# Performance work log

Hardware: AMD Instinct MI355X
Metric: run time of the kernel (lower is better)

The kernel has to match this reference:

```python
import jax, jax.numpy as jnp
import numpy as np

N_NODES = 100000
N_EDGES = 3200000
BN_EPS = 1e-5


def setup_inputs() -> dict:
    key = jax.random.key(0)
    ks = jax.random.split(key, 16)
    return {
        "x": jax.random.normal(ks[0], (N_NODES, 2), jnp.float32),
        "eq_labels": jax.random.randint(ks[1], (N_NODES,), 0, 32, jnp.int32),
        "edge_index": jax.random.randint(ks[2], (2, N_EDGES), 0, N_NODES, jnp.int32),
        "eq_emb": jax.random.normal(ks[3], (32, 8), jnp.float32),
        "W1_0": jax.random.normal(ks[4], (10, 64), jnp.float32) * 0.3,
        "b1_0": jnp.zeros((64,), jnp.float32),
        "W2_0": jax.random.normal(ks[5], (64, 64), jnp.float32) * 0.12,
        "b2_0": jnp.zeros((64,), jnp.float32),
        "eps_0": jnp.zeros((), jnp.float32),
        "gamma_0": jnp.ones((64,), jnp.float32),
        "beta_0": jnp.zeros((64,), jnp.float32),
        "W1_s": jax.random.normal(ks[6], (2, 64, 64), jnp.float32) * 0.12,
        "b1_s": jnp.zeros((2, 64), jnp.float32),
        "W2_s": jax.random.normal(ks[7], (2, 64, 64), jnp.float32) * 0.12,
        "b2_s": jnp.zeros((2, 64), jnp.float32),
        "eps_s": jnp.zeros((2,), jnp.float32),
        "gamma_s": jnp.ones((2, 64), jnp.float32),
        "beta_s": jnp.zeros((2, 64), jnp.float32),
        "Wf": jax.random.normal(ks[8], (64, 1), jnp.float32) * 0.12,
        "bf": jnp.zeros((1,), jnp.float32),
    }


def _gin_bn_relu(h, src, dst, W1, b1, W2, b2, eps, gamma, beta):
    # GINConv: (1+eps)*x_i + sum_{j->i} x_j, then 2-layer ReLU MLP, then BN, ReLU
    agg = jax.ops.segment_sum(h[src], dst, num_segments=N_NODES)
    h = (1.0 + eps) * h + agg
    h = jax.nn.relu(h @ W1 + b1)
    h = jax.nn.relu(h @ W2 + b2)
    mu = jnp.mean(h, axis=0)
    var = jnp.var(h, axis=0)
    h = (h - mu) * jax.lax.rsqrt(var + BN_EPS) * gamma + beta
    return jax.nn.relu(h)


def reference(x, eq_labels, edge_index, eq_emb, W1_0, b1_0, W2_0, b2_0, eps_0,
              gamma_0, beta_0, W1_s, b1_s, W2_s, b2_s, eps_s, gamma_s, beta_s,
              Wf, bf):
    src, dst = edge_index[0], edge_index[1]
    h = jnp.concatenate([x, eq_emb[eq_labels]], axis=-1)  # [N, 10]
    h = _gin_bn_relu(h, src, dst, W1_0, b1_0, W2_0, b2_0, eps_0, gamma_0, beta_0)
    for i in range(2):
        h = _gin_bn_relu(h, src, dst, W1_s[i], b1_s[i], W2_s[i], b2_s[i],
                         eps_s[i], gamma_s[i], beta_s[i])
    return (h @ Wf + bf).squeeze(-1)  # [N]
```

## Files before the change

### kernel.cpp

```cpp
#include <hip/hip_runtime.h>

#define N_NODES 100000
#define N_EDGES 3200000
#define BN_EPS 1e-5f

#define BLK_NODES 128
#define NBLK 782
#define CHUNK 16384
#define NW ((N_EDGES + CHUNK - 1) / CHUNK)
#define BCAP 4480
#define CUR_PAD 16
#define NSLICE 32

typedef unsigned int uint;
typedef unsigned short ushort;
typedef _Float16 half_t;
typedef __attribute__((ext_vector_type(8))) _Float16 h8v;
typedef __attribute__((ext_vector_type(4))) float f4v;

__device__ inline float bf_lo(uint u) { return __uint_as_float(u << 16); }
__device__ inline float bf_hi(uint u) { return __uint_as_float(u & 0xffff0000u); }
__device__ inline float h_lo(uint u) {
    union { ushort s; half_t h; } r; r.s = (ushort)(u & 0xffffu); return (float)r.h;
}
__device__ inline float h_hi(uint u) {
    union { ushort s; half_t h; } r; r.s = (ushort)(u >> 16); return (float)r.h;
}
__device__ inline ushort f2bf(float a) {
    uint ua = __float_as_uint(a); ua += 0x7fffu + ((ua >> 16) & 1u);
    return (ushort)(ua >> 16);
}
__device__ inline ushort f2h(float a) {
    union { half_t h; ushort u; } r;
    r.h = (half_t)a;
    return r.u;
}
__device__ inline uint packh2(float a, float b) {
    return (uint)f2h(a) | ((uint)f2h(b) << 16);
}
__device__ inline h8v loadH(const ushort* p) {
    union { uint4 q; h8v f; } r;
    r.q = *(const uint4*)p;
    return r.f;
}
__device__ inline h8v loadHh(const half_t* p) {
    union { uint4 q; h8v f; } r;
    r.q = *(const uint4*)p;
    return r.f;
}
__device__ inline f4v mfma16(h8v a, h8v b, f4v c) {
    return __builtin_amdgcn_mfma_f32_16x16x32_f16(a, b, c, 0, 0, 0);
}

#define FETCH_COLS(rr, st, dg, mx, wv, wv2)                                   \
    {                                                                         \
        int _r = (rr);                                                        \
        st = __shfl(myStart, 2 * _r + hl, 64);                                \
        dg = __shfl(myDeg, 2 * _r + hl, 64);                                  \
        int _dA = __shfl(myDeg, 2 * _r, 64);                                  \
        int _dB = __shfl(myDeg, 2 * _r + 1, 64);                              \
        mx = max(_dA, _dB);                                                   \
        int _e1 = min(l5, dg - 1); _e1 = _e1 < 0 ? 0 : _e1;                   \
        int _e2 = min(32 + l5, dg - 1); _e2 = _e2 < 0 ? 0 : _e2;              \
        wv = col[st + _e1];                                                   \
        wv2 = col[st + _e2];                                                  \
    }

__global__ __launch_bounds__(256) void k_h0(const float* __restrict__ x,
                                            const int* __restrict__ lab,
                                            const float* __restrict__ emb,
                                            ushort* __restrict__ h0,
                                            const float* __restrict__ W1_0,
                                            const float* __restrict__ W2_0,
                                            const float* __restrict__ W1_s,
                                            const float* __restrict__ W2_s,
                                            ushort* __restrict__ W0t,
                                            ushort* __restrict__ W20t,
                                            ushort* __restrict__ Wst, int n) {
    int i = blockIdx.x * blockDim.x + threadIdx.x;
    if (i < n) {
        float v[16];
        v[0] = x[2 * i];
        v[1] = x[2 * i + 1];
        int L = lab[i];
#pragma unroll
        for (int k = 0; k < 8; k++) v[2 + k] = emb[L * 8 + k];
#pragma unroll
        for (int k = 10; k < 16; k++) v[k] = 0.f;
        uint o8[8];
#pragma unroll
        for (int k = 0; k < 8; k++) o8[k] = packh2(v[2 * k], v[2 * k + 1]);
        uint4* o = (uint4*)(h0 + (size_t)i * 16);
        o[0] = uint4{o8[0], o8[1], o8[2], o8[3]};
        o[1] = uint4{o8[4], o8[5], o8[6], o8[7]};
    }
    if (blockIdx.x == 0) {
        int t = threadIdx.x;
        for (int j = t; j < 64 * 32; j += 256) {
            int nn = j >> 5, k = j & 31;
            W0t[j] = (k < 10) ? f2h(W1_0[k * 64 + nn]) : (ushort)0;
        }
        for (int j = t; j < 4096; j += 256) {
            int nn = j >> 6, k = j & 63;
            W20t[j] = f2h(W2_0[k * 64 + nn]);
        }
        for (int l = 0; l < 2; l++) {
            const float* w1 = W1_s + l * 4096;
            const float* w2 = W2_s + l * 4096;
            for (int j = t; j < 4096; j += 256) {
                int nn = j >> 6, k = j & 63;
                Wst[l * 8192 + j] = f2h(w1[k * 64 + nn]);
                Wst[l * 8192 + 4096 + j] = f2h(w2[k * 64 + nn]);
            }
        }
    }
}

__global__ __launch_bounds__(256) void k_fill(const int* __restrict__ src,
                                              const int* __restrict__ dst,
                                              int* __restrict__ gcur,
                                              int* __restrict__ bucket) {
    __shared__ int cnt[NBLK];
    __shared__ int off[NBLK];
    int t = threadIdx.x;
    for (int b = t; b < NBLK; b += 256) cnt[b] = 0;
    __syncthreads();
    int my0 = blockIdx.x * CHUNK + t * 64;
    for (int k = 0; k < 64; k += 4) {
        int e = my0 + k;
        if (e + 3 < N_EDGES) {
            int4 d4 = *(const int4*)(dst + e);
            atomicAdd(&cnt[d4.x >> 7], 1);
            atomicAdd(&cnt[d4.y >> 7], 1);
            atomicAdd(&cnt[d4.z >> 7], 1);
            atomicAdd(&cnt[d4.w >> 7], 1);
        } else {
#pragma unroll
            for (int kk = 0; kk < 4; kk++) {
                int ee = e + kk;
                if (ee < N_EDGES) atomicAdd(&cnt[dst[ee] >> 7], 1);
            }
        }
    }
    __syncthreads();
    for (int b = t; b < NBLK; b += 256) {
        int c = cnt[b];
        off[b] = (c > 0) ? atomicAdd(&gcur[b * CUR_PAD], c) : 0;
    }
    __syncthreads();
    for (int k = 0; k < 64; k += 4) {
        int e = my0 + k;
        if (e + 3 < N_EDGES) {
            int4 d4 = *(const int4*)(dst + e);
            int4 s4 = *(const int4*)(src + e);
            int dd[4] = {d4.x, d4.y, d4.z, d4.w};
            int ss[4] = {s4.x, s4.y, s4.z, s4.w};
#pragma unroll
            for (int kk = 0; kk < 4; kk++) {
                int b = dd[kk] >> 7;
                int p = atomicAdd(&off[b], 1);
                if (p < BCAP)
                    bucket[(size_t)b * BCAP + p] = ((dd[kk] & 127) << 17) | ss[kk];
            }
        } else {
#pragma unroll
            for (int kk = 0; kk < 4; kk++) {
                int ee = e + kk;
                if (ee < N_EDGES) {
                    int d = dst[ee], s = src[ee];
                    int b = d >> 7;
                    int p = atomicAdd(&off[b], 1);
                    if (p < BCAP)
                        bucket[(size_t)b * BCAP + p] = ((d & 127) << 17) | s;
                }
            }
        }
    }
}

__global__ __launch_bounds__(256) void k_sort(const int* __restrict__ gcur,
                                              const int* __restrict__ bucket,
                                              int* __restrict__ col2,
                                              int2* __restrict__ nodeoff, int n) {
    __shared__ int cnt[BLK_NODES];
    __shared__ int scn[BLK_NODES];
    __shared__ int cur[BLK_NODES];
    int t = threadIdx.x;
    int blk = blockIdx.x;
    if (t < BLK_NODES) cnt[t] = 0;
    __syncthreads();
    int cc = min(gcur[blk * CUR_PAD], BCAP);
    const int* bb = bucket + (size_t)blk * BCAP;
    for (int i = t; i < cc; i += 256) atomicAdd(&cnt[bb[i] >> 17], 1);
    __syncthreads();
    if (t < BLK_NODES) scn[t] = cnt[t];
    __syncthreads();
#pragma unroll
    for (int off = 1; off < BLK_NODES; off <<= 1) {
        int v = (t >= off && t < BLK_NODES) ? scn[t - off] : 0;
        __syncthreads();
        if (t < BLK_NODES) scn[t] += v;
        __syncthreads();
    }
    if (t < BLK_NODES) {
        int start = scn[t] - cnt[t];
        cur[t] = start;
        int node = blk * BLK_NODES + t;
        if (node < n) nodeoff[node] = int2{blk * BCAP + start, cnt[t]};
    }
    __syncthreads();
    int* out = col2 + (size_t)blk * BCAP;
    for (int i = t; i < cc; i += 256) {
        int w = bb[i];
        int p = atomicAdd(&cur[w >> 17], 1);
        out[p] = w & 0x1FFFF;
    }
}

__global__ __launch_bounds__(256, 4) void k_layer0M(const ushort* __restrict__ h0,
                                                    const int2* __restrict__ nodeoff,
                                                    const int* __restrict__ col,
                                                    const float* __restrict__ epsp,
                                                    const ushort* __restrict__ W0t,
                                                    const float* __restrict__ b1,
                                                    const ushort* __restrict__ W20t,
                                                    const float* __restrict__ b2,
                                                    ushort* __restrict__ hraw,
                                                    float* __restrict__ part_out) {
    __shared__ half_t buf[4][16][72];
    int t = threadIdx.x, w = t >> 6, lane = t & 63;
    int base = blockIdx.x * 64 + w * 16;
    float ep = 1.f + *epsp;
    int hl = lane >> 5, l5 = lane & 31;
    int q = l5 & 3, g = l5 >> 2;
    const uint* hb = (const uint*)h0;

    int nj = base + (lane & 15);
    int2 no2 = nodeoff[nj];
    bool njv = nj < N_NODES;
    int myStart = njv ? no2.x : 0;
    int myDeg = njv ? no2.y : 0;

    int stC, dgC, mxC, wvC, wv2C;
    int stN, dgN, mxN, wvN, wv2N;
    FETCH_COLS(0, stC, dgC, mxC, wvC, wv2C);
    FETCH_COLS(1, stN, dgN, mxN, wvN, wv2N);

    for (int r = 0; r < 8; r++) {
        int stNN, dgNN, mxNN, wvNN, wv2NN;
        FETCH_COLS(min(r + 2, 7), stNN, dgNN, mxNN, wvNN, wv2NN);
        int deg = dgC, mx = mxC;
        float ac[4] = {0.f, 0.f, 0.f, 0.f};
        if (mx > 0) {
            int idx[4];
#pragma unroll
            for (int i = 0; i < 4; i++) idx[i] = __shfl(wvC, (hl << 5) + g + 8 * i, 64);
            uint2 rows[4];
#pragma unroll
            for (int i = 0; i < 4; i++)
                rows[i] = *(const uint2*)(hb + (size_t)idx[i] * 8 + q * 2);
#pragma unroll
            for (int i = 0; i < 4; i++) {
                float m = (g + 8 * i < deg) ? 1.f : 0.f;
                ac[0] = fmaf(m, h_lo(rows[i].x), ac[0]);
                ac[1] = fmaf(m, h_hi(rows[i].x), ac[1]);
                ac[2] = fmaf(m, h_lo(rows[i].y), ac[2]);
                ac[3] = fmaf(m, h_hi(rows[i].y), ac[3]);
            }
            if (mx > 32) {
                int idx2[4];
#pragma unroll
                for (int i = 0; i < 4; i++) idx2[i] = __shfl(wv2C, (hl << 5) + g + 8 * i, 64);
                uint2 rows2[4];
#pragma unroll
                for (int i = 0; i < 4; i++)
                    rows2[i] = *(const uint2*)(hb + (size_t)idx2[i] * 8 + q * 2);
#pragma unroll
                for (int i = 0; i < 4; i++) {
                    float m = (32 + g + 8 * i < deg) ? 1.f : 0.f;
                    ac[0] = fmaf(m, h_lo(rows2[i].x), ac[0]);
                    ac[1] = fmaf(m, h_hi(rows2[i].x), ac[1]);
                    ac[2] = fmaf(m, h_lo(rows2[i].y), ac[2]);
                    ac[3] = fmaf(m, h_hi(rows2[i].y), ac[3]);
                }
                for (int e = 64 + g; e < deg; e += 8) {
                    uint2 v = *(const uint2*)(hb + (size_t)col[stC + e] * 8 + q * 2);
                    ac[0] += h_lo(v.x); ac[1] += h_hi(v.x);
                    ac[2] += h_lo(v.y); ac[3] += h_hi(v.y);
                }
            }
        }
#pragma unroll
        for (int o = 4; o < 32; o <<= 1) {
#pragma unroll
            for (int k = 0; k < 4; k++) ac[k] += __shfl_xor(ac[k], o, 64);
        }
        int node = base + 2 * r + hl;
        bool valid = node < N_NODES;
        int nodeC = valid ? node : 0;
        float vm = valid ? ep : 0.f;
        uint2 sv = *(const uint2*)(hb + (size_t)nodeC * 8 + q * 2);
        ac[0] = fmaf(vm, h_lo(sv.x), ac[0]);
        ac[1] = fmaf(vm, h_hi(sv.x), ac[1]);
        ac[2] = fmaf(vm, h_lo(sv.y), ac[2]);
        ac[3] = fmaf(vm, h_hi(sv.y), ac[3]);
        if (!valid) { ac[0] = ac[1] = ac[2] = ac[3] = 0.f; }
        if (g == 0) {
            int nl = 2 * r + hl;
            *(uint2*)&buf[w][nl][q * 4] = uint2{packh2(ac[0], ac[1]), packh2(ac[2], ac[3])};
            *(uint2*)&buf[w][nl][16 + q * 4] = uint2{0u, 0u};
        }
        stC = stN; dgC = dgN; mxC = mxN; wvC = wvN; wv2C = wv2N;
        stN = stNN; dgN = dgNN; mxN = mxNN; wvN = wvNN; wv2N = wv2NN;
    }
    int mr = lane & 15, kq = lane >> 4, nc = lane & 15;
    h8v A0 = loadHh(&buf[w][mr][kq * 8]);
#pragma unroll
    for (int nt = 0; nt < 4; nt++) {
        float bb = b1[nt * 16 + nc];
        f4v c = {bb, bb, bb, bb};
        c = mfma16(A0, loadH(W0t + (nt * 16 + nc) * 32 + kq * 8), c);
#pragma unroll
        for (int r2 = 0; r2 < 4; r2++)
            buf[w][kq * 4 + r2][nt * 16 + nc] = (half_t)fmaxf(c[r2], 0.f);
    }
    h8v P0 = loadHh(&buf[w][mr][kq * 8]);
    h8v P1 = loadHh(&buf[w][mr][32 + kq * 8]);
    float sA[4], sB[4];
#pragma unroll
    for (int nt = 0; nt < 4; nt++) { sA[nt] = 0.f; sB[nt] = 0.f; }
#pragma unroll
    for (int nt = 0; nt < 4; nt++) {
        float bb = b2[nt * 16 + nc];
        f4v c = {bb, bb, bb, bb};
        c = mfma16(P0, loadH(W20t + (nt * 16 + nc) * 64 + kq * 8), c);
        c = mfma16(P1, loadH(W20t + (nt * 16 + nc) * 64 + 32 + kq * 8), c);
#pragma unroll
        for (int r2 = 0; r2 < 4; r2++) {
            int node = base + kq * 4 + r2;
            float vv = fmaxf(c[r2], 0.f);
            if (node < N_NODES) {
                sA[nt] += vv;
                sB[nt] = fmaf(vv, vv, sB[nt]);
                hraw[(size_t)node * 64 + nt * 16 + nc] = f2h(vv);
            }
        }
    }
#pragma unroll
    for (int o = 16; o < 64; o <<= 1) {
#pragma unroll
        for (int nt = 0; nt < 4; nt++) {
            sA[nt] += __shfl_xor(sA[nt], o, 64);
            sB[nt] += __shfl_xor(sB[nt], o, 64);
        }
    }
    if (kq == 0) {
        float* pp = part_out + (blockIdx.x & (NSLICE - 1)) * 128;
#pragma unroll
        for (int nt = 0; nt < 4; nt++) {
            atomicAdd(&pp[nt * 16 + nc], sA[nt]);
            atomicAdd(&pp[64 + nt * 16 + nc], sB[nt]);
        }
    }
}

__global__ __launch_bounds__(256) void k_act(const ushort* __restrict__ hraw,
                                             const float* __restrict__ part,
                                             const float* __restrict__ gamma,
                                             const float* __restrict__ beta,
                                             ushort* __restrict__ act, float invn) {
    __shared__ float st[128];
    __shared__ float sc[64], sh[64];
    int t = threadIdx.x;
    if (t < 128) {
        float S = 0.f;
#pragma unroll 8
        for (int s = 0; s < NSLICE; s++) S += part[s * 128 + t];
        st[t] = S;
    }
    __syncthreads();
    if (t < 64) {
        float mu = st[t] * invn;
        float var = fmaxf(st[64 + t] * invn - mu * mu, 0.f);
        float s = gamma[t] * rsqrtf(var + BN_EPS);
        sc[t] = s;
        sh[t] = beta[t] - mu * s;
    }
    __syncthreads();
    int base = (blockIdx.x * 256 + t) * 4;
    int f0 = base & 63;
    uint2 hv = *(const uint2*)(hraw + base);
    float a0 = fmaxf(fmaf(h_lo(hv.x), sc[f0 + 0], sh[f0 + 0]), 0.f);
    float a1 = fmaxf(fmaf(h_hi(hv.x), sc[f0 + 1], sh[f0 + 1]), 0.f);
    float a2 = fmaxf(fmaf(h_lo(hv.y), sc[f0 + 2], sh[f0 + 2]), 0.f);
    float a3 = fmaxf(fmaf(h_hi(hv.y), sc[f0 + 3], sh[f0 + 3]), 0.f);
    uint2 o;
    o.x = packh2(a0, a1);
    o.y = packh2(a2, a3);
    *(uint2*)(act + base) = o;
}

__global__ __launch_bounds__(256, 6) void k_layerM(const uint* __restrict__ actin,
                                                   const int2* __restrict__ nodeoff,
                                                   const int* __restrict__ col,
                                                   const float* __restrict__ epsp,
                                                   const ushort* __restrict__ W1t,
                                                   const float* __restrict__ b1,
                                                   const ushort* __restrict__ W2t,
                                                   const float* __restrict__ b2,
                                                   ushort* __restrict__ hraw,
                                                   float* __restrict__ part_out) {
    __shared__ ushort stg[4][2048];
    __shared__ half_t buf[4][16][72];
    int t = threadIdx.x, w = t >> 6, lane = t & 63;
    int wbase = blockIdx.x * 64 + w * 16;
    float ep = 1.f + *epsp;
    int nc = lane & 15, kq = lane >> 4;
    const ushort* au = (const ushort*)actin;

    int nj = wbase + nc;
    int2 no2 = nodeoff[nj];
    bool njv = nj < N_NODES;
    int sm = njv ? no2.x : 0;
    int dm = njv ? no2.y : 0;
    int se = sm + dm;

    int e0 = __shfl(sm, 0, 64);
    int eEnd = __shfl(se, 15, 64);
    e0 = max(0, min(e0, NBLK * BCAP - 1));
    int T = max(eEnd - e0, 0);
    int eLast = min(e0 + max(T - 1, 0), NBLK * BCAP - 1);
    int C = min((max(T, 1) + 31) >> 5, (BCAP + 31) >> 5);

    f4v acc[4];
#pragma unroll
    for (int nt = 0; nt < 4; nt++) {
#pragma unroll
        for (int r = 0; r < 4; r++) {
            int nd = wbase + kq * 4 + r;
            float vm = (nd < N_NODES) ? ep : 0.f;
            int ndc = (nd < N_NODES) ? nd : 0;
            acc[nt][r] = vm * h_lo(au[(size_t)ndc * 64 + nt * 16 + nc]);
        }
    }

    int s5 = lane & 31, hh = lane >> 5;
    char* tb = (char*)&stg[w][0];
    char* lw = tb + s5 * 32 + hh * 16;
    uint rdaddr = (uint)(size_t)tb + (uint)(kq * 256 + nc * 8);

    int colv = min(col[min(e0 + s5, eLast)] & 0x1FFFF, N_NODES - 1);

    for (int j = 0; j < C; j++) {
        const ushort* gs = au + (size_t)colv * 64 + hh * 8;
        uint4 rv0 = *(const uint4*)(gs);
        uint4 rv1 = *(const uint4*)(gs + 16);
        uint4 rv2 = *(const uint4*)(gs + 32);
        uint4 rv3 = *(const uint4*)(gs + 48);
        int ci = min(e0 + (j + 1) * 32 + s5, eLast);
        int colvN = min(col[ci] & 0x1FFFF, N_NODES - 1);
        *(uint4*)(lw) = rv0;
        *(uint4*)(lw + 1024) = rv1;
        *(uint4*)(lw + 2048) = rv2;
        *(uint4*)(lw + 3072) = rv3;
        int eb = e0 + j * 32 + kq * 8;
        union { uint u[4]; h8v v; } aw;
#pragma unroll
        for (int p = 0; p < 4; p++) {
            int ea = eb + 2 * p;
            uint lo = (ea >= sm && ea < se) ? 0x3C00u : 0u;
            uint hi = (ea + 1 >= sm && ea + 1 < se) ? 0x3C000000u : 0u;
            aw.u[p] = lo | hi;
        }
        uint2 p0, p1, p2, p3, p4, p5, p6, p7;
        asm volatile(
            "ds_read_b64_tr_b16 %0, %8 offset:0\n\t"
            "ds_read_b64_tr_b16 %1, %8 offset:128\n\t"
            "ds_read_b64_tr_b16 %2, %8 offset:1024\n\t"
            "ds_read_b64_tr_b16 %3, %8 offset:1152\n\t"
            "ds_read_b64_tr_b16 %4, %8 offset:2048\n\t"
            "ds_read_b64_tr_b16 %5, %8 offset:2176\n\t"
            "ds_read_b64_tr_b16 %6, %8 offset:3072\n\t"
            "ds_read_b64_tr_b16 %7, %8 offset:3200\n\t"
            "s_waitcnt lgkmcnt(0)"
            : "=&v"(p0), "=&v"(p1), "=&v"(p2), "=&v"(p3),
              "=&v"(p4), "=&v"(p5), "=&v"(p6), "=&v"(p7)
            : "v"(rdaddr)
            : "memory");
        __builtin_amdgcn_sched_barrier(0);
        union { uint2 q[2]; h8v v; } b0, b1v, b2v, b3;
        b0.q[0] = p0;  b0.q[1] = p1;
        b1v.q[0] = p2; b1v.q[1] = p3;
        b2v.q[0] = p4; b2v.q[1] = p5;
        b3.q[0] = p6;  b3.q[1] = p7;
        acc[0] = mfma16(aw.v, b0.v, acc[0]);
        acc[1] = mfma16(aw.v, b1v.v, acc[1]);
        acc[2] = mfma16(aw.v, b2v.v, acc[2]);
        acc[3] = mfma16(aw.v, b3.v, acc[3]);
        colv = colvN;
    }

#pragma unroll
    for (int nt = 0; nt < 4; nt++) {
#pragma unroll
        for (int r2 = 0; r2 < 4; r2++)
            buf[w][kq * 4 + r2][nt * 16 + nc] = (half_t)acc[nt][r2];
    }

    int mr = lane & 15;
    h8v A0 = loadHh(&buf[w][mr][kq * 8]);
    h8v A1 = loadHh(&buf[w][mr][32 + kq * 8]);
#pragma unroll
    for (int nt = 0; nt < 4; nt++) {
        float bb = b1[nt * 16 + nc];
        f4v c = {bb, bb, bb, bb};
        c = mfma16(A0, loadH(W1t + (nt * 16 + nc) * 64 + kq * 8), c);
        c = mfma16(A1, loadH(W1t + (nt * 16 + nc) * 64 + 32 + kq * 8), c);
#pragma unroll
        for (int r2 = 0; r2 < 4; r2++)
            buf[w][kq * 4 + r2][nt * 16 + nc] = (half_t)fmaxf(c[r2], 0.f);
    }
    h8v P0 = loadHh(&buf[w][mr][kq * 8]);
    h8v P1 = loadHh(&buf[w][mr][32 + kq * 8]);
    float sA[4], sB[4];
#pragma unroll
    for (int nt = 0; nt < 4; nt++) { sA[nt] = 0.f; sB[nt] = 0.f; }
#pragma unroll
    for (int nt = 0; nt < 4; nt++) {
        float bb = b2[nt * 16 + nc];
        f4v c = {bb, bb, bb, bb};
        c = mfma16(P0, loadH(W2t + (nt * 16 + nc) * 64 + kq * 8), c);
        c = mfma16(P1, loadH(W2t + (nt * 16 + nc) * 64 + 32 + kq * 8), c);
#pragma unroll
        for (int r2 = 0; r2 < 4; r2++) {
            int node = wbase + kq * 4 + r2;
            float vv = fmaxf(c[r2], 0.f);
            if (node < N_NODES) {
                sA[nt] += vv;
                sB[nt] = fmaf(vv, vv, sB[nt]);
                hraw[(size_t)node * 64 + nt * 16 + nc] = f2h(vv);
            }
        }
    }
#pragma unroll
    for (int o = 16; o < 64; o <<= 1) {
#pragma unroll
        for (int nt = 0; nt < 4; nt++) {
            sA[nt] += __shfl_xor(sA[nt], o, 64);
            sB[nt] += __shfl_xor(sB[nt], o, 64);
        }
    }
    if (kq == 0) {
        float* pp = part_out + (blockIdx.x & (NSLICE - 1)) * 128;
#pragma unroll
        for (int nt = 0; nt < 4; nt++) {
            atomicAdd(&pp[nt * 16 + nc], sA[nt]);
            atomicAdd(&pp[64 + nt * 16 + nc], sB[nt]);
        }
    }
}

__global__ __launch_bounds__(256) void k_out(const ushort* __restrict__ hraw,
                                             const float* __restrict__ part,
                                             const float* __restrict__ gamma,
                                             const float* __restrict__ beta,
                                             const float* __restrict__ Wf,
                                             const float* __restrict__ bfp,
                                             float* __restrict__ out, int n,
                                             float invn) {
    __shared__ float st[128];
    __shared__ float sc[64], sh[64];
    int t = threadIdx.x;
    if (t < 128) {
        float S = 0.f;
#pragma unroll 8
        for (int s = 0; s < NSLICE; s++) S += part[s * 128 + t];
        st[t] = S;
    }
    __syncthreads();
    if (t < 64) {
        float mu = st[t] * invn;
        float var = fmaxf(st[64 + t] * invn - mu * mu, 0.f);
        float s = gamma[t] * rsqrtf(var + BN_EPS);
        sc[t] = s;
        sh[t] = beta[t] - mu * s;
    }
    __syncthreads();
    int i = blockIdx.x * blockDim.x + threadIdx.x;
    if (i >= n) return;
    float acc = *bfp;
    const uint2* h2 = (const uint2*)(hraw + (size_t)i * 64);
#pragma unroll
    for (int qq = 0; qq < 16; qq++) {
        uint2 v = h2[qq];
        int j = qq * 4;
        acc = fmaf(fmaxf(fmaf(h_lo(v.x), sc[j + 0], sh[j + 0]), 0.f), Wf[j + 0], acc);
        acc = fmaf(fmaxf(fmaf(h_hi(v.x), sc[j + 1], sh[j + 1]), 0.f), Wf[j + 1], acc);
        acc = fmaf(fmaxf(fmaf(h_lo(v.y), sc[j + 2], sh[j + 2]), 0.f), Wf[j + 2], acc);
        acc = fmaf(fmaxf(fmaf(h_hi(v.y), sc[j + 3], sh[j + 3]), 0.f), Wf[j + 3], acc);
    }
    out[i] = acc;
}

extern "C" void kernel_launch(void* const* d_in, const int* in_sizes, int n_in,
                              void* d_out, int out_size, void* d_ws, size_t ws_size,
                              hipStream_t stream) {
    const float* x      = (const float*)d_in[0];
    const int*   lab    = (const int*)d_in[1];
    const int*   edge   = (const int*)d_in[2];
    const float* emb    = (const float*)d_in[3];
    const float* W1_0   = (const float*)d_in[4];
    const float* b1_0   = (const float*)d_in[5];
    const float* W2_0   = (const float*)d_in[6];
    const float* b2_0   = (const float*)d_in[7];
    const float* eps_0  = (const float*)d_in[8];
    const float* gamma_0= (const float*)d_in[9];
    const float* beta_0 = (const float*)d_in[10];
    const float* W1_s   = (const float*)d_in[11];
    const float* b1_s   = (const float*)d_in[12];
    const float* W2_s   = (const float*)d_in[13];
    const float* b2_s   = (const float*)d_in[14];
    const float* eps_s  = (const float*)d_in[15];
    const float* gamma_s= (const float*)d_in[16];
    const float* beta_s = (const float*)d_in[17];
    const float* Wf     = (const float*)d_in[18];
    const float* bf     = (const float*)d_in[19];

    const int N = N_NODES, E = N_EDGES;
    const int* srcp = edge;
    const int* dstp = edge + E;

    char* p = (char*)d_ws;
    auto alloc = [&](size_t bytes) {
        void* r = (void*)p;
        p += (bytes + 255) & ~(size_t)255;
        return r;
    };
    int* bucket  = (int*)alloc((size_t)NBLK * BCAP * 4);
    int* col2    = (int*)alloc((size_t)NBLK * BCAP * 4);
    int* gcur    = (int*)alloc((size_t)NBLK * CUR_PAD * 4);
    int* nodeoff = (int*)alloc((size_t)(N + 64) * 8);
    ushort* hraw = (ushort*)alloc((size_t)N * 64 * 2);
    ushort* act  = (ushort*)alloc((size_t)N * 64 * 2);
    ushort* h0   = (ushort*)alloc((size_t)N * 16 * 2);
    float* parts = (float*)alloc(3 * NSLICE * 128 * 4);
    ushort* W0t  = (ushort*)alloc(64 * 32 * 2);
    ushort* W20t = (ushort*)alloc(4096 * 2);
    ushort* Wst  = (ushort*)alloc(2 * 8192 * 2);

    hipMemsetAsync(gcur, 0, (size_t)NBLK * CUR_PAD * 4, stream);
    hipMemsetAsync(parts, 0, 3 * NSLICE * 128 * 4, stream);
    hipMemsetAsync(nodeoff + 2 * (size_t)N, 0, 64 * 8, stream);

    const int TB = 256;
    const int gN = (N + TB - 1) / TB;
    const int gM = (N + 63) / 64;
    const int gA = N * 64 / 1024;
    const float invn = 1.0f / (float)N;

    k_h0<<<gN, TB, 0, stream>>>(x, lab, emb, h0, W1_0, W2_0, W1_s, W2_s,
                                W0t, W20t, Wst, N);
    k_fill<<<NW, TB, 0, stream>>>(srcp, dstp, gcur, bucket);
    k_sort<<<NBLK, TB, 0, stream>>>(gcur, bucket, col2, (int2*)nodeoff, N);

    k_layer0M<<<gM, TB, 0, stream>>>(h0, (const int2*)nodeoff, col2, eps_0, W0t,
                                     b1_0, W20t, b2_0, hraw,
                                     parts + 0 * NSLICE * 128);
    k_act<<<gA, TB, 0, stream>>>(hraw, parts + 0 * NSLICE * 128, gamma_0, beta_0,
                                 act, invn);

    k_layerM<<<gM, TB, 0, stream>>>((const uint*)act, (const int2*)nodeoff, col2,
                                    eps_s + 0, Wst + 0 * 8192, b1_s + 0 * 64,
                                    Wst + 0 * 8192 + 4096, b2_s + 0 * 64,
                                    hraw, parts + 1 * NSLICE * 128);
    k_act<<<gA, TB, 0, stream>>>(hraw, parts + 1 * NSLICE * 128, gamma_s + 0 * 64,
                                 beta_s + 0 * 64, act, invn);

    k_layerM<<<gM, TB, 0, stream>>>((const uint*)act, (const int2*)nodeoff, col2,
                                    eps_s + 1, Wst + 1 * 8192, b1_s + 1 * 64,
                                    Wst + 1 * 8192 + 4096, b2_s + 1 * 64,
                                    hraw, parts + 2 * NSLICE * 128);

    k_out<<<gN, TB, 0, stream>>>(hraw, parts + 2 * NSLICE * 128,
                                 gamma_s + 1 * 64, beta_s + 1 * 64, Wf, bf,
                                 (float*)d_out, N, invn);
}
```

Measured before the change: 405.4 us.

## Deepen gather prefetch pipeline to two rows ahead in layer aggregation loop

```diff
diff --git a/kernel.cpp b/kernel.cpp
--- a/kernel.cpp
+++ b/kernel.cpp
@@ -400,7 +400,7 @@
     *(uint2*)(act + base) = o;
 }
 
-__global__ __launch_bounds__(256, 6) void k_layerM(const uint* __restrict__ actin,
+__global__ __launch_bounds__(256, 4) void k_layerM(const uint* __restrict__ actin,
                                                    const int2* __restrict__ nodeoff,
                                                    const int* __restrict__ col,
                                                    const float* __restrict__ epsp,
@@ -449,20 +449,40 @@
     char* lw = tb + s5 * 32 + hh * 16;
     uint rdaddr = (uint)(size_t)tb + (uint)(kq * 256 + nc * 8);
 
-    int colv = min(col[min(e0 + s5, eLast)] & 0x1FFFF, N_NODES - 1);
+    int c0 = min(col[min(e0 + s5, eLast)] & 0x1FFFF, N_NODES - 1);
+    int c1 = min(col[min(e0 + 32 + s5, eLast)] & 0x1FFFF, N_NODES - 1);
+    int c2 = min(col[min(e0 + 64 + s5, eLast)] & 0x1FFFF, N_NODES - 1);
+    uint4 a0, a1, a2, a3, b0v, b1v, b2v, b3v;
+    {
+        const ushort* gs = au + (size_t)c0 * 64 + hh * 8;
+        a0 = *(const uint4*)(gs);
+        a1 = *(const uint4*)(gs + 16);
+        a2 = *(const uint4*)(gs + 32);
+        a3 = *(const uint4*)(gs + 48);
+    }
+    {
+        const ushort* gs = au + (size_t)c1 * 64 + hh * 8;
+        b0v = *(const uint4*)(gs);
+        b1v = *(const uint4*)(gs + 16);
+        b2v = *(const uint4*)(gs + 32);
+        b3v = *(const uint4*)(gs + 48);
+    }
 
     for (int j = 0; j < C; j++) {
-        const ushort* gs = au + (size_t)colv * 64 + hh * 8;
-        uint4 rv0 = *(const uint4*)(gs);
-        uint4 rv1 = *(const uint4*)(gs + 16);
-        uint4 rv2 = *(const uint4*)(gs + 32);
-        uint4 rv3 = *(const uint4*)(gs + 48);
-        int ci = min(e0 + (j + 1) * 32 + s5, eLast);
-        int colvN = min(col[ci] & 0x1FFFF, N_NODES - 1);
-        *(uint4*)(lw) = rv0;
-        *(uint4*)(lw + 1024) = rv1;
-        *(uint4*)(lw + 2048) = rv2;
-        *(uint4*)(lw + 3072) = rv3;
+        *(uint4*)(lw) = a0;
+        *(uint4*)(lw + 1024) = a1;
+        *(uint4*)(lw + 2048) = a2;
+        *(uint4*)(lw + 3072) = a3;
+        uint4 n0, n1, n2, n3;
+        {
+            const ushort* gs = au + (size_t)c2 * 64 + hh * 8;
+            n0 = *(const uint4*)(gs);
+            n1 = *(const uint4*)(gs + 16);
+            n2 = *(const uint4*)(gs + 32);
+            n3 = *(const uint4*)(gs + 48);
+        }
+        c2 = min(col[min(e0 + (j + 3) * 32 + s5, eLast)] & 0x1FFFF, N_NODES - 1);
+        __builtin_amdgcn_sched_barrier(0);
         int eb = e0 + j * 32 + kq * 8;
         union { uint u[4]; h8v v; } aw;
 #pragma unroll
@@ -488,16 +508,17 @@
             : "v"(rdaddr)
             : "memory");
         __builtin_amdgcn_sched_barrier(0);
-        union { uint2 q[2]; h8v v; } b0, b1v, b2v, b3;
-        b0.q[0] = p0;  b0.q[1] = p1;
-        b1v.q[0] = p2; b1v.q[1] = p3;
-        b2v.q[0] = p4; b2v.q[1] = p5;
-        b3.q[0] = p6;  b3.q[1] = p7;
-        acc[0] = mfma16(aw.v, b0.v, acc[0]);
-        acc[1] = mfma16(aw.v, b1v.v, acc[1]);
-        acc[2] = mfma16(aw.v, b2v.v, acc[2]);
-        acc[3] = mfma16(aw.v, b3.v, acc[3]);
-        colv = colvN;
+        union { uint2 q[2]; h8v v; } f0, f1, f2, f3;
+        f0.q[0] = p0; f0.q[1] = p1;
+        f1.q[0] = p2; f1.q[1] = p3;
+        f2.q[0] = p4; f2.q[1] = p5;
+        f3.q[0] = p6; f3.q[1] = p7;
+        acc[0] = mfma16(aw.v, f0.v, acc[0]);
+        acc[1] = mfma16(aw.v, f1.v, acc[1]);
+        acc[2] = mfma16(aw.v, f2.v, acc[2]);
+        acc[3] = mfma16(aw.v, f3.v, acc[3]);
+        a0 = b0v; a1 = b1v; a2 = b2v; a3 = b3v;
+        b0v = n0; b1v = n1; b2v = n2; b3v = n3;
     }
 
 #pragma unroll
```

Result: no change. 411.3 us (+1.5%).
